# Performance work log

Measured on AMD Instinct MI355X. Metric: run time of the kernel, lower is better.

## Reference

```python
import jax, jax.numpy as jnp
import numpy as np

N = 2048      # nodes: 8 sequences x 256 tokens
E = 524288    # edges: dense attention graph, 8 * 256^2
H = 8         # heads
DK = 64       # per-head dim


def setup_inputs() -> dict:
    key = jax.random.key(0)
    k1, k2, k3, k4, k5 = jax.random.split(key, 5)
    q = jax.random.normal(k1, (N, H, DK), dtype=jnp.float32)
    k = jax.random.normal(k2, (N, H, DK), dtype=jnp.float32)
    v = jax.random.normal(k3, (N, H, DK), dtype=jnp.float32)
    edge_src = jax.random.randint(k4, (E,), 0, N, dtype=jnp.int32)
    edge_dst = jax.random.randint(k5, (E,), 0, N, dtype=jnp.int32)
    return {"q": q, "k": k, "v": v, "edge_src": edge_src, "edge_dst": edge_dst}


def reference(q, k, v, edge_src, edge_dst):
    # src_dot_dst('k','q','score'): per-edge dot product over head dim -> [E, H]
    score = jnp.einsum('ehd,ehd->eh', k[edge_src], q[edge_dst])
    # scaled_exp('score', sqrt(d_k)): exp(clamp(score / sqrt(d_k), -10, 10))
    score = jnp.exp(jnp.clip(score / jnp.sqrt(jnp.float32(DK)), -10.0, 10.0))
    # send_and_recv: wv = sum_dst(v_src * score), z = sum_dst(score)
    wv = jax.ops.segment_sum(v[edge_src] * score[:, :, None], edge_dst, num_segments=N)  # [N, H, DK]
    z = jax.ops.segment_sum(score, edge_dst, num_segments=N)  # [N, H]
    # post_func normalization: attention output per node
    return wv / z[:, :, None]
```

## Files before the change

### kernel.cpp

```cpp
#include <hip/hip_runtime.h>

#define NNODES 2048
#define NHEAD 8
#define DKDIM 64

typedef unsigned int uint;
typedef unsigned short ushort;
typedef unsigned char uchar;
typedef __fp16 h2 __attribute__((ext_vector_type(2)));
typedef __fp16 h8 __attribute__((ext_vector_type(8)));
typedef float f16v __attribute__((ext_vector_type(16)));

#define KSCALE 0.18033688011112042f
#define CLAMP2 14.426950408889634f

__device__ __forceinline__ uint pk2(float a, float b) {
    union { h2 h; uint u; } x; x.h = __builtin_amdgcn_cvt_pkrtz(a, b); return x.u;
}

__global__ void prep12(const float* __restrict__ k, const float* __restrict__ v,
                       uint4* __restrict__ kc4, uint4* __restrict__ vt4,
                       uint4* __restrict__ A4) {
    __shared__ float tile[64][65];
    int b = blockIdx.x, t = threadIdx.x;
    if (b < 512) {
        int i = b * 256 + t;
        int f = i >> 6, l = i & 63;
        int jq = f & 3, sr = (f >> 2) & 1, ts = (f >> 3) & 31, h = f >> 8;
        int node = ts * 64 + sr * 32 + (l & 31);
        int dim0 = (2 * jq + (l >> 5)) * 8;
        const float* src = k + (size_t)node * 512 + h * 64 + dim0;
        float4 f0 = *(const float4*)src;
        float4 f1 = *(const float4*)(src + 4);
        uint4 o;
        o.x = pk2(f0.x * KSCALE, f0.y * KSCALE);
        o.y = pk2(f0.z * KSCALE, f0.w * KSCALE);
        o.z = pk2(f1.x * KSCALE, f1.y * KSCALE);
        o.w = pk2(f1.z * KSCALE, f1.w * KSCALE);
        kc4[(size_t)f * 64 + l] = o;
    } else if (b < 768) {
        int bv = b - 512;
        int h = bv & 7, tn = bv >> 3;
        int nl = t >> 2, dq = (t & 3) * 16;
        const float* src = v + (size_t)(tn * 64 + nl) * 512 + h * 64 + dq;
#pragma unroll
        for (int i = 0; i < 4; ++i) {
            float4 f = *(const float4*)(src + i * 4);
            tile[nl][dq + i * 4 + 0] = f.x;
            tile[nl][dq + i * 4 + 1] = f.y;
            tile[nl][dq + i * 4 + 2] = f.z;
            tile[nl][dq + i * 4 + 3] = f.w;
        }
        __syncthreads();
#pragma unroll
        for (int rep = 0; rep < 2; ++rep) {
            int slot = rep * 256 + t;
            int fsub = slot >> 6, l = slot & 63;
            int srv = fsub >> 2, ks = (fsub >> 1) & 1, dg = fsub & 1;
            int dim = dg * 32 + (l & 31);
            int s8 = (srv * 4 + ks * 2 + (l >> 5)) * 8;
            uint4 o;
            o.x = pk2(tile[s8 + 0][dim], tile[s8 + 1][dim]);
            o.y = pk2(tile[s8 + 2][dim], tile[s8 + 3][dim]);
            o.z = pk2(tile[s8 + 4][dim], tile[s8 + 5][dim]);
            o.w = pk2(tile[s8 + 6][dim], tile[s8 + 7][dim]);
            int fV = (h * 32 + tn) * 8 + srv * 4 + ks * 2 + dg;
            vt4[(size_t)fV * 64 + l] = o;
        }
    } else {
        uint4 zz = {0u, 0u, 0u, 0u};
        A4[(size_t)(b - 768) * 512 + t] = zz;
        A4[(size_t)(b - 768) * 512 + t + 256] = zz;
    }
}

__global__ void histA(const int* __restrict__ es, const int* __restrict__ ed,
                      uint* __restrict__ A32, int E) {
    int i = blockIdx.x * 256 + threadIdx.x;
    if (i < E) {
        uint idx = (uint)ed[i] * 2048u + (uint)es[i];
        atomicAdd(&A32[idx >> 3], 1u << ((idx & 7) * 4));
    }
}

__global__ void __launch_bounds__(512, 2) attn_kernel(
    const float* __restrict__ q, const char* __restrict__ kc, const char* __restrict__ vt,
    const uchar* __restrict__ A8, float* __restrict__ out) {
    __shared__ float CL[64 * 68];
    __shared__ float CLz[64];

    int b = blockIdx.x;
    int j = b & 7, idx = b >> 3;
    int dt = (j & 3) * 8 + (idx >> 2);
    int h = (j >> 2) * 4 + (idx & 3);
    int dst0 = dt * 64;
    int t = threadIdx.x;
    int w = t >> 6, half = w >> 2;
    int u = w & 3, sr = u >> 1, dc = u & 1;
    int l = t & 63, lm = l & 31, hi = l >> 5;

    int ts0 = half * 16;
    const char* kBase = kc + ((size_t)(h * 32 + ts0) * 8 + sr * 4) * 1024 + l * 16;
    const char* vBase = vt + ((size_t)(h * 32 + ts0) * 8 + sr * 4) * 1024 + l * 16;
    const char* aRow = (const char*)A8 + (size_t)(dst0 + dc * 32 + lm) * 1024 + sr * 16
                       + ts0 * 32;

    h8 qf[4];
    {
        const float* qp = q + (size_t)(dst0 + dc * 32 + lm) * 512 + h * 64 + hi * 8;
#pragma unroll
        for (int jq = 0; jq < 4; ++jq) {
            float4 f0 = *(const float4*)(qp + jq * 16);
            float4 f1 = *(const float4*)(qp + jq * 16 + 4);
            union { uint u4[4]; h8 v; } U;
            U.u4[0] = pk2(f0.x, f0.y); U.u4[1] = pk2(f0.z, f0.w);
            U.u4[2] = pk2(f1.x, f1.y); U.u4[3] = pk2(f1.z, f1.w);
            qf[jq] = U.v;
        }
    }

    f16v of[2];
#pragma unroll
    for (int dg = 0; dg < 2; ++dg)
#pragma unroll
        for (int i = 0; i < 16; ++i) of[dg][i] = 0.f;
    float z = 0.f;

    uint4 kcur[4], knxt[4], vcur[4];
    uint4 ac, an;

#pragma unroll
    for (int jq = 0; jq < 4; ++jq)
        kcur[jq] = *(const uint4*)(kBase + jq * 1024);
    ac = *(const uint4*)aRow;

    for (int it = 0; it < 16; ++it) {
        size_t toff = (size_t)it * 8192;
#pragma unroll
        for (int ks = 0; ks < 2; ++ks)
#pragma unroll
            for (int dg = 0; dg < 2; ++dg)
                vcur[ks * 2 + dg] = *(const uint4*)(vBase + toff + (ks * 2 + dg) * 1024);
        int itn = (it < 15) ? it + 1 : it;
        an = *(const uint4*)(aRow + itn * 32);

        f16v sacc;
#pragma unroll
        for (int i = 0; i < 16; ++i) sacc[i] = 0.f;
        __builtin_amdgcn_s_setprio(1);
#pragma unroll
        for (int jq = 0; jq < 4; ++jq) {
            union { uint4 u; h8 v; } KF; KF.u = kcur[jq];
            sacc = __builtin_amdgcn_mfma_f32_32x32x16_f16(KF.v, qf[jq], sacc, 0, 0, 0);
        }
        __builtin_amdgcn_s_setprio(0);

#pragma unroll
        for (int jq = 0; jq < 4; ++jq)
            knxt[jq] = *(const uint4*)(kBase + (size_t)itn * 8192 + jq * 1024);

        uint W[4][2];
        {
            const uint* aw4 = (const uint*)&ac;
#pragma unroll
            for (int G = 0; G < 4; ++G) {
                uint aw = aw4[G];
                float ee[4];
#pragma unroll
                for (int j2 = 0; j2 < 4; ++j2) {
                    float sc = fminf(fmaxf(sacc[4 * G + j2], -CLAMP2), CLAMP2);
                    ee[j2] = exp2f(sc) * (float)((aw >> (16 * hi + 4 * j2)) & 15u);
                    z += ee[j2];
                }
                W[G][0] = pk2(ee[0], ee[1]);
                W[G][1] = pk2(ee[2], ee[3]);
            }
        }
        uint Wx[4][2];
#pragma unroll
        for (int G = 0; G < 4; ++G) {
            Wx[G][0] = __shfl_xor(W[G][0], 32);
            Wx[G][1] = __shfl_xor(W[G][1], 32);
        }

        __builtin_amdgcn_s_setprio(1);
#pragma unroll
        for (int ks = 0; ks < 2; ++ks) {
            union { uint u4[4]; h8 v; } S;
            S.u4[0] = hi ? Wx[2 * ks + 1][0] : W[2 * ks][0];
            S.u4[1] = hi ? Wx[2 * ks + 1][1] : W[2 * ks][1];
            S.u4[2] = hi ? W[2 * ks + 1][0] : Wx[2 * ks][0];
            S.u4[3] = hi ? W[2 * ks + 1][1] : Wx[2 * ks][1];
#pragma unroll
            for (int dg = 0; dg < 2; ++dg) {
                union { uint4 u; h8 v; } VF; VF.u = vcur[ks * 2 + dg];
                of[dg] = __builtin_amdgcn_mfma_f32_32x32x16_f16(VF.v, S.v, of[dg], 0, 0, 0);
            }
        }
        __builtin_amdgcn_s_setprio(0);

#pragma unroll
        for (int jq = 0; jq < 4; ++jq) kcur[jq] = knxt[jq];
        ac = an;
    }

    z += __shfl_xor(z, 32);

    int gid = half * 2 + sr;
    for (int p = 0; p < 4; ++p) {
        if (gid == p) {
#pragma unroll
            for (int dg = 0; dg < 2; ++dg)
#pragma unroll
                for (int reg = 0; reg < 16; ++reg) {
                    int dim = dg * 32 + (reg & 3) + 8 * (reg >> 2) + 4 * hi;
                    int idx2 = (dc * 32 + lm) * 68 + dim;
                    if (p == 0) CL[idx2] = of[dg][reg];
                    else CL[idx2] += of[dg][reg];
                }
            if (hi == 0) {
                if (p == 0) CLz[dc * 32 + lm] = z;
                else CLz[dc * 32 + lm] += z;
            }
        }
        __syncthreads();
    }

    {
        int dst = t >> 3, d8 = t & 7;
        float inv = 1.0f / CLz[dst];
        float4 o0 = *(float4*)(CL + dst * 68 + d8 * 8);
        float4 o1 = *(float4*)(CL + dst * 68 + d8 * 8 + 4);
        o0.x *= inv; o0.y *= inv; o0.z *= inv; o0.w *= inv;
        o1.x *= inv; o1.y *= inv; o1.z *= inv; o1.w *= inv;
        float* op = out + (size_t)(dst0 + dst) * 512 + h * 64 + d8 * 8;
        *(float4*)op = o0;
        *(float4*)(op + 4) = o1;
    }
}


extern "C" void kernel_launch(void* const* d_in, const int* in_sizes, int n_in,
                              void* d_out, int out_size, void* d_ws, size_t ws_size,
                              hipStream_t stream) {
    const float* q = (const float*)d_in[0];
    const float* k = (const float*)d_in[1];
    const float* v = (const float*)d_in[2];
    const int* esrc = (const int*)d_in[3];
    const int* edst = (const int*)d_in[4];
    float* out = (float*)d_out;
    const int E = in_sizes[3];

    uchar* A8 = (uchar*)d_ws;
    char* kc = (char*)(A8 + (size_t)NNODES * NNODES / 2);
    char* vt = kc + (size_t)NHEAD * NNODES * DKDIM * 2;

    prep12<<<1024, 256, 0, stream>>>(k, v, (uint4*)kc, (uint4*)vt, (uint4*)A8);
    histA<<<(E + 255) / 256, 256, 0, stream>>>(esrc, edst, (uint*)A8, E);
    attn_kernel<<<256, 512, 0, stream>>>(q, kc, vt, A8, out);
}
```

Measured before the change: 55.49 us.

## Tile adjacency counts for coalesced loads and unroll attention loop by two

The 4-bit edge-count adjacency matrix is stored in a tiled layout, so each lane's per-iteration uint4 load of the count matrix becomes contiguous across lanes instead of striding by 1024 bytes per row. The main attention loop now handles two 32-source tiles per iteration, with two independent score accumulators and double-buffered K/V/adjacency loads, which gives more instruction-level parallelism between MFMA, exp and memory work. The cost is higher register pressure under launch_bounds(512,2), which could cause spills or reduce overlap.

```diff
diff --git a/kernel.cpp b/kernel.cpp
--- a/kernel.cpp
+++ b/kernel.cpp
@@ -78,8 +78,10 @@
                       uint* __restrict__ A32, int E) {
     int i = blockIdx.x * 256 + threadIdx.x;
     if (i < E) {
-        uint idx = (uint)ed[i] * 2048u + (uint)es[i];
-        atomicAdd(&A32[idx >> 3], 1u << ((idx & 7) * 4));
+        uint s = (uint)es[i], d = (uint)ed[i];
+        uint uidx = ((d >> 6) << 14) + ((s >> 6) << 9) + (((s >> 5) & 1u) << 8) +
+                    (((d >> 5) & 1u) << 7) + ((d & 31u) << 2) + ((s >> 3) & 3u);
+        atomicAdd(&A32[uidx], 1u << ((s & 7u) << 2));
     }
 }
 
@@ -102,8 +104,8 @@
     int ts0 = half * 16;
     const char* kBase = kc + ((size_t)(h * 32 + ts0) * 8 + sr * 4) * 1024 + l * 16;
     const char* vBase = vt + ((size_t)(h * 32 + ts0) * 8 + sr * 4) * 1024 + l * 16;
-    const char* aRow = (const char*)A8 + (size_t)(dst0 + dc * 32 + lm) * 1024 + sr * 16
-                       + ts0 * 32;
+    const char* aRow = (const char*)A8 + (size_t)dt * 65536 + (size_t)ts0 * 2048 +
+                       sr * 1024 + dc * 512 + lm * 16;
 
     h8 qf[4];
     {
@@ -126,82 +128,104 @@
         for (int i = 0; i < 16; ++i) of[dg][i] = 0.f;
     float z = 0.f;
 
-    uint4 kcur[4], knxt[4], vcur[4];
-    uint4 ac, an;
-
-#pragma unroll
-    for (int jq = 0; jq < 4; ++jq)
-        kcur[jq] = *(const uint4*)(kBase + jq * 1024);
-    ac = *(const uint4*)aRow;
-
-    for (int it = 0; it < 16; ++it) {
-        size_t toff = (size_t)it * 8192;
-#pragma unroll
-        for (int ks = 0; ks < 2; ++ks)
-#pragma unroll
-            for (int dg = 0; dg < 2; ++dg)
-                vcur[ks * 2 + dg] = *(const uint4*)(vBase + toff + (ks * 2 + dg) * 1024);
-        int itn = (it < 15) ? it + 1 : it;
-        an = *(const uint4*)(aRow + itn * 32);
-
-        f16v sacc;
-#pragma unroll
-        for (int i = 0; i < 16; ++i) sacc[i] = 0.f;
+    uint4 k0f[4], k1f[4], v0f[4], v1f[4];
+    uint4 ac0, ac1;
+
+#pragma unroll
+    for (int f = 0; f < 4; ++f) {
+        k0f[f] = *(const uint4*)(kBase + f * 1024);
+        k1f[f] = *(const uint4*)(kBase + 8192 + f * 1024);
+    }
+    ac0 = *(const uint4*)aRow;
+    ac1 = *(const uint4*)(aRow + 2048);
+
+    for (int p = 0; p < 8; ++p) {
+        int r0t = 2 * p, r1t = 2 * p + 1;
+        size_t o0 = (size_t)r0t * 8192, o1 = (size_t)r1t * 8192;
+#pragma unroll
+        for (int f = 0; f < 4; ++f) {
+            v0f[f] = *(const uint4*)(vBase + o0 + f * 1024);
+            v1f[f] = *(const uint4*)(vBase + o1 + f * 1024);
+        }
+
+        f16v sacc0, sacc1;
+#pragma unroll
+        for (int i = 0; i < 16; ++i) { sacc0[i] = 0.f; sacc1[i] = 0.f; }
         __builtin_amdgcn_s_setprio(1);
 #pragma unroll
         for (int jq = 0; jq < 4; ++jq) {
-            union { uint4 u; h8 v; } KF; KF.u = kcur[jq];
-            sacc = __builtin_amdgcn_mfma_f32_32x32x16_f16(KF.v, qf[jq], sacc, 0, 0, 0);
+            union { uint4 u; h8 v; } KF; KF.u = k0f[jq];
+            sacc0 = __builtin_amdgcn_mfma_f32_32x32x16_f16(KF.v, qf[jq], sacc0, 0, 0, 0);
+        }
+#pragma unroll
+        for (int jq = 0; jq < 4; ++jq) {
+            union { uint4 u; h8 v; } KF; KF.u = k1f[jq];
+            sacc1 = __builtin_amdgcn_mfma_f32_32x32x16_f16(KF.v, qf[jq], sacc1, 0, 0, 0);
         }
         __builtin_amdgcn_s_setprio(0);
 
-#pragma unroll
-        for (int jq = 0; jq < 4; ++jq)
-            knxt[jq] = *(const uint4*)(kBase + (size_t)itn * 8192 + jq * 1024);
-
-        uint W[4][2];
+        int n0 = (p < 7) ? r0t + 2 : r0t;
+        int n1 = (p < 7) ? r1t + 2 : r1t;
+#pragma unroll
+        for (int f = 0; f < 4; ++f) {
+            k0f[f] = *(const uint4*)(kBase + (size_t)n0 * 8192 + f * 1024);
+            k1f[f] = *(const uint4*)(kBase + (size_t)n1 * 8192 + f * 1024);
+        }
+
+        uint W0[4][2], W1[4][2];
         {
-            const uint* aw4 = (const uint*)&ac;
+            const uint* a0 = (const uint*)&ac0;
+            const uint* a1 = (const uint*)&ac1;
 #pragma unroll
             for (int G = 0; G < 4; ++G) {
-                uint aw = aw4[G];
-                float ee[4];
+                float e0[4], e1[4];
 #pragma unroll
                 for (int j2 = 0; j2 < 4; ++j2) {
-                    float sc = fminf(fmaxf(sacc[4 * G + j2], -CLAMP2), CLAMP2);
-                    ee[j2] = exp2f(sc) * (float)((aw >> (16 * hi + 4 * j2)) & 15u);
-                    z += ee[j2];
+                    float s0 = fminf(fmaxf(sacc0[4 * G + j2], -CLAMP2), CLAMP2);
+                    float s1 = fminf(fmaxf(sacc1[4 * G + j2], -CLAMP2), CLAMP2);
+                    e0[j2] = exp2f(s0) * (float)((a0[G] >> (16 * hi + 4 * j2)) & 15u);
+                    e1[j2] = exp2f(s1) * (float)((a1[G] >> (16 * hi + 4 * j2)) & 15u);
+                    z += e0[j2] + e1[j2];
                 }
-                W[G][0] = pk2(ee[0], ee[1]);
-                W[G][1] = pk2(ee[2], ee[3]);
+                W0[G][0] = pk2(e0[0], e0[1]); W0[G][1] = pk2(e0[2], e0[3]);
+                W1[G][0] = pk2(e1[0], e1[1]); W1[G][1] = pk2(e1[2], e1[3]);
             }
         }
-        uint Wx[4][2];
+
+        ac0 = *(const uint4*)(aRow + (size_t)n0 * 2048);
+        ac1 = *(const uint4*)(aRow + (size_t)n1 * 2048);
+
+        uint Wx0[4][2], Wx1[4][2];
 #pragma unroll
         for (int G = 0; G < 4; ++G) {
-            Wx[G][0] = __shfl_xor(W[G][0], 32);
-            Wx[G][1] = __shfl_xor(W[G][1], 32);
+            Wx0[G][0] = __shfl_xor(W0[G][0], 32);
+            Wx0[G][1] = __shfl_xor(W0[G][1], 32);
+            Wx1[G][0] = __shfl_xor(W1[G][0], 32);
+            Wx1[G][1] = __shfl_xor(W1[G][1], 32);
         }
 
         __builtin_amdgcn_s_setprio(1);
 #pragma unroll
         for (int ks = 0; ks < 2; ++ks) {
-            union { uint u4[4]; h8 v; } S;
-            S.u4[0] = hi ? Wx[2 * ks + 1][0] : W[2 * ks][0];
-            S.u4[1] = hi ? Wx[2 * ks + 1][1] : W[2 * ks][1];
-            S.u4[2] = hi ? W[2 * ks + 1][0] : Wx[2 * ks][0];
-            S.u4[3] = hi ? W[2 * ks + 1][1] : Wx[2 * ks][1];
+            union { uint u4[4]; h8 v; } S0, S1;
+            S0.u4[0] = hi ? Wx0[2 * ks + 1][0] : W0[2 * ks][0];
+            S0.u4[1] = hi ? Wx0[2 * ks + 1][1] : W0[2 * ks][1];
+            S0.u4[2] = hi ? W0[2 * ks + 1][0] : Wx0[2 * ks][0];
+            S0.u4[3] = hi ? W0[2 * ks + 1][1] : Wx0[2 * ks][1];
+            S1.u4[0] = hi ? Wx1[2 * ks + 1][0] : W1[2 * ks][0];
+            S1.u4[1] = hi ? Wx1[2 * ks + 1][1] : W1[2 * ks][1];
+            S1.u4[2] = hi ? W1[2 * ks + 1][0] : Wx1[2 * ks][0];
+            S1.u4[3] = hi ? W1[2 * ks + 1][1] : Wx1[2 * ks][1];
 #pragma unroll
             for (int dg = 0; dg < 2; ++dg) {
-                union { uint4 u; h8 v; } VF; VF.u = vcur[ks * 2 + dg];
-                of[dg] = __builtin_amdgcn_mfma_f32_32x32x16_f16(VF.v, S.v, of[dg], 0, 0, 0);
+                union { uint4 u; h8 v; } VF0, VF1;
+                VF0.u = v0f[ks * 2 + dg];
+                VF1.u = v1f[ks * 2 + dg];
+                of[dg] = __builtin_amdgcn_mfma_f32_32x32x16_f16(VF0.v, S0.v, of[dg], 0, 0, 0);
+                of[dg] = __builtin_amdgcn_mfma_f32_32x32x16_f16(VF1.v, S1.v, of[dg], 0, 0, 0);
             }
         }
         __builtin_amdgcn_s_setprio(0);
-
-#pragma unroll
-        for (int jq = 0; jq < 4; ++jq) kcur[jq] = knxt[jq];
-        ac = an;
     }
 
     z += __shfl_xor(z, 32);
```

Result: no change. 55.45 us, median of 2 (-0.1%).
